# Kernel tuning notes

Hardware: AMD Instinct MI355X
Metric: run time of the kernel (lower is better)

The kernel has to match this reference:

```python
import jax, jax.numpy as jnp
import numpy as np

NUM_HEADS = 12
HEAD_DIM = 64
NPT = 1  # num_prefix_tokens

def _rot(x):
    # pairs (x0,x1) -> (-x1, x0), matching timm's rot()
    x2 = x.reshape(*x.shape[:-1], -1, 2)
    r = jnp.stack([-x2[..., 1], x2[..., 0]], axis=-1)
    return r.reshape(x.shape)

def _apply_rope_cat(x, rope):
    # rope: [N_rot, 2*hd] = sin||cos concatenated
    sin, cos = jnp.split(rope, 2, axis=-1)
    return x * cos + _rot(x) * sin

def setup_inputs() -> dict:
    key = jax.random.key(0)
    ks = jax.random.split(key, 7)
    B, N, C = 8, 4097, 768
    hd = HEAD_DIM
    x = jax.random.normal(ks[0], (B, N, C), jnp.float32)
    rope = jax.random.normal(ks[1], (N - NPT, 2 * hd), jnp.float32)
    qkv_w = jax.random.normal(ks[2], (3 * C, C), jnp.float32) * (C ** -0.5)
    q_bias = jax.random.normal(ks[3], (C,), jnp.float32) * 0.02
    v_bias = jax.random.normal(ks[4], (C,), jnp.float32) * 0.02
    proj_w = jax.random.normal(ks[5], (C, C), jnp.float32) * (C ** -0.5)
    proj_b = jax.random.normal(ks[6], (C,), jnp.float32) * 0.02
    return dict(x=x, rope=rope, qkv_w=qkv_w, q_bias=q_bias, v_bias=v_bias,
                proj_w=proj_w, proj_b=proj_b)

def reference(x, rope, qkv_w, q_bias, v_bias, proj_w, proj_b):
    B, N, C = x.shape
    H, hd = NUM_HEADS, HEAD_DIM
    # fused QKV with k_bias fixed at zero (non-trainable buffer)
    bias = jnp.concatenate([q_bias, jnp.zeros_like(q_bias), v_bias])
    qkv = x @ qkv_w.T + bias                            # [B,N,3C]
    qkv = qkv.reshape(B, N, 3, H, hd).transpose(2, 0, 3, 1, 4)
    q, k, v = qkv[0], qkv[1], qkv[2]                    # [B,H,N,hd]
    # RoPE on all tokens except the prefix (CLS) token
    q = jnp.concatenate([q[:, :, :NPT], _apply_rope_cat(q[:, :, NPT:], rope)], axis=2)
    k = jnp.concatenate([k[:, :, :NPT], _apply_rope_cat(k[:, :, NPT:], rope)], axis=2)
    # linear attention: kv = K^T V, then Q @ kv, normalized by hd*N
    kv = jnp.einsum('bhnd,bhne->bhde', k, v)            # [B,H,hd,hd]
    out = jnp.einsum('bhnd,bhde->bhne', q, kv) / hd / N # [B,H,N,hd]
    out = out.transpose(0, 2, 1, 3).reshape(B, N, C)
    return out @ proj_w.T + proj_b
```

## Files before the change

kernel.cpp:

```cpp
#include <hip/hip_runtime.h>
#include <hip/hip_bf16.h>

typedef __attribute__((ext_vector_type(8))) short short8;
typedef __attribute__((ext_vector_type(4))) float f32x4;

#define B_    8
#define N_    4097
#define C_    768
#define M_TOT (B_*N_)
#define K3    (3*C_)
#define CHUNKS 16
#define NSTEP 24

__device__ __forceinline__ float bf2f(unsigned short u) {
  union { unsigned int i; float f; } x; x.i = ((unsigned int)u) << 16; return x.f;
}
__device__ __forceinline__ unsigned short f2bf(float f) {
  union { float f; unsigned int i; } x; x.f = f;
  unsigned int i = x.i + 0x7fffu + ((x.i >> 16) & 1u);
  return (unsigned short)(i >> 16);
}
__device__ __forceinline__ void gload16(const void* g, void* l) {
  __builtin_amdgcn_global_load_lds(
      (const __attribute__((address_space(1))) void*)g,
      (__attribute__((address_space(3))) void*)l, 16, 0, 0);
}

__global__ __launch_bounds__(256) void cvt_kernel(const float* __restrict__ inx,
                                                  unsigned short* __restrict__ outx,
                                                  const float* __restrict__ inw,
                                                  unsigned short* __restrict__ outw,
                                                  long n4x, long n4tot) {
  long i = (long)blockIdx.x * blockDim.x + threadIdx.x;
  long stride = (long)gridDim.x * blockDim.x;
  for (; i < n4tot; i += stride) {
    const float4* src; ushort4* dst; long j;
    if (i < n4x) { src = (const float4*)inx; dst = (ushort4*)outx; j = i; }
    else         { src = (const float4*)inw; dst = (ushort4*)outw; j = i - n4x; }
    float4 v = src[j];
    ushort4 o;
    o.x = f2bf(v.x); o.y = f2bf(v.y); o.z = f2bf(v.z); o.w = f2bf(v.w);
    dst[j] = o;
  }
}

__global__ __launch_bounds__(512, 4) void gemm_qkv_rope(
    const unsigned short* __restrict__ A,
    const unsigned short* __restrict__ Bw,
    const float* __restrict__ rope,
    const float* __restrict__ qb,
    const float* __restrict__ vb,
    unsigned short* __restrict__ qkv)
{
  __shared__ __align__(16) char L[3*24576];
  const int tid  = threadIdx.x;
  const int wave = tid >> 6, lane = tid & 63;
  const int lr = lane & 15, lk = lane >> 4;
  const int wm = wave >> 2, wn = wave & 3;

  const int o = blockIdx.x;
  const int xcd = o & 7, loc = o >> 3;
  const int tile = (xcd < 1 ? xcd*290 : 290 + (xcd-1)*289) + loc;
  const int m0 = (tile % 257) * 128;
  const int n0 = (tile / 257) * 256;

  const int arow = tid >> 2, achk = tid & 3;
  const int am = min(m0 + arow, M_TOT-1);
  const unsigned short* gA  = A  + (long)am*768 + achk*8;
  const unsigned short* gB1 = Bw + (long)(n0 + arow)*768 + achk*8;
  const unsigned short* gB2 = Bw + (long)(n0 + arow + 128)*768 + achk*8;
  const int dA  = wave*1024;
  const int dB1 = 8192  + wave*1024;
  const int dB2 = 16384 + wave*1024;

  const int abase = (wm*64 + lr)*64 + lk*16;
  const int bbase = 8192 + (wn*64 + lr)*64 + lk*16;

  f32x4 acc[4][4];
#pragma unroll
  for (int i = 0; i < 4; ++i)
#pragma unroll
    for (int j = 0; j < 4; ++j) acc[i][j] = (f32x4){0.f,0.f,0.f,0.f};

  auto STAGE = [&](int buf, int kk) {
    char* sb = L + buf*24576;
    gload16(gA  + kk, sb + dA);
    gload16(gB1 + kk, sb + dB1);
    gload16(gB2 + kk, sb + dB2);
  };
  auto COMPUTE = [&](int buf) {
    const char* sb = L + buf*24576;
    short8 af[4], bfr[4];
#pragma unroll
    for (int mi = 0; mi < 4; ++mi)
      af[mi] = *(const short8*)(sb + abase + mi*1024);
#pragma unroll
    for (int ni = 0; ni < 4; ++ni)
      bfr[ni] = *(const short8*)(sb + bbase + ni*1024);
#pragma unroll
    for (int mi = 0; mi < 4; ++mi)
#pragma unroll
      for (int ni = 0; ni < 4; ++ni)
        acc[mi][ni] = __builtin_amdgcn_mfma_f32_16x16x32_bf16(af[mi], bfr[ni], acc[mi][ni], 0, 0, 0);
  };

  STAGE(0, 0);
  STAGE(1, 32);
  asm volatile("s_waitcnt vmcnt(3)" ::: "memory");
  __builtin_amdgcn_s_barrier();
  __builtin_amdgcn_sched_barrier(0);

  int cur = 0;
  for (int tt = 0; tt < NSTEP-2; ++tt) {
    int stg = cur + 2; if (stg >= 3) stg -= 3;
    STAGE(stg, (tt+2)*32);
    COMPUTE(cur);
    asm volatile("s_waitcnt vmcnt(3)" ::: "memory");
    __builtin_amdgcn_sched_barrier(0);
    __builtin_amdgcn_s_barrier();
    __builtin_amdgcn_sched_barrier(0);
    cur = (cur + 1 == 3) ? 0 : cur + 1;
  }
  COMPUTE(cur);
  asm volatile("s_waitcnt vmcnt(0)" ::: "memory");
  __builtin_amdgcn_sched_barrier(0);
  __builtin_amdgcn_s_barrier();
  __builtin_amdgcn_sched_barrier(0);
  cur = (cur + 1 == 3) ? 0 : cur + 1;
  COMPUTE(cur);

  const int which = n0 / 768;
  unsigned short* plane = qkv + (long)which*M_TOT*768;

  float biasv[4]; int withv[4]; int dv[4];
#pragma unroll
  for (int ni = 0; ni < 4; ++ni) {
    const int gc = n0 + wn*64 + ni*16 + lr;
    const int within = gc - which*768;
    withv[ni] = within;
    dv[ni] = within & 63;
    biasv[ni] = (which == 0) ? qb[within] : (which == 2 ? vb[within] : 0.f);
  }

  if (which == 2) {
#pragma unroll
    for (int mi = 0; mi < 4; ++mi)
#pragma unroll
      for (int r = 0; r < 4; ++r) {
        const int gm = m0 + wm*64 + mi*16 + lk*4 + r;
        if (gm < M_TOT) {
#pragma unroll
          for (int ni = 0; ni < 4; ++ni)
            plane[(long)gm*768 + withv[ni]] = f2bf(acc[mi][ni][r] + biasv[ni]);
        }
      }
  } else {
#pragma unroll
    for (int mi = 0; mi < 4; ++mi) {
#pragma unroll
      for (int r = 0; r < 4; ++r) {
        const int gm = m0 + wm*64 + mi*16 + lk*4 + r;
        const int ntok = gm % 4097;
        const bool valid = gm < M_TOT;
        const bool dorope = (ntok > 0) && valid;
        const float* rp = rope + (long)(ntok - 1)*128;
#pragma unroll
        for (int ni = 0; ni < 4; ++ni) {
          float v = acc[mi][ni][r] + biasv[ni];
          float pair = __shfl_xor(v, 1);
          float vo = v;
          if (dorope) {
            const float s = rp[dv[ni]], c = rp[64 + dv[ni]];
            const float rot = (dv[ni] & 1) ? pair : -pair;
            vo = v*c + rot*s;
          }
          if (valid) plane[(long)gm*768 + withv[ni]] = f2bf(vo);
        }
      }
    }
  }
}

__global__ __launch_bounds__(256) void kv_partial_kernel(
    const unsigned short* __restrict__ qkv, float* __restrict__ part)
{
  const int bh = blockIdx.y;
  const int b = bh / 12, h = bh % 12;
  const int chunk = blockIdx.x;
  const int per = (N_ + CHUNKS - 1) / CHUNKS;
  const int nst = chunk * per;
  const int nen = min(nst + per, N_);
  const unsigned short* Kpl = qkv + (long)M_TOT*768 + ((long)b*N_)*768 + h*64;
  const unsigned short* Vpl = qkv + (long)2*M_TOT*768 + ((long)b*N_)*768 + h*64;
  __shared__ unsigned short Kl[32*64];
  __shared__ unsigned short Vl[32*64];
  const int t = threadIdx.x;
  const int ty = t >> 4, tx = t & 15;
  const int lrow = t >> 3, lpc = t & 7;
  float acc[4][4] = {};
  for (int nb = nst; nb < nen; nb += 32) {
    const int cnt = min(32, nen - nb);
    __syncthreads();
    if (lrow < cnt) {
      *(uint4*)(Kl + lrow*64 + lpc*8) = *(const uint4*)(Kpl + (long)(nb + lrow)*768 + lpc*8);
      *(uint4*)(Vl + lrow*64 + lpc*8) = *(const uint4*)(Vpl + (long)(nb + lrow)*768 + lpc*8);
    }
    __syncthreads();
#pragma unroll 2
    for (int i = 0; i < cnt; ++i) {
      const ushort4 ku = *(const ushort4*)(Kl + i*64 + ty*4);
      const ushort4 vu = *(const ushort4*)(Vl + i*64 + tx*4);
      float kf[4] = {bf2f(ku.x), bf2f(ku.y), bf2f(ku.z), bf2f(ku.w)};
      float vf[4] = {bf2f(vu.x), bf2f(vu.y), bf2f(vu.z), bf2f(vu.w)};
#pragma unroll
      for (int a = 0; a < 4; ++a)
#pragma unroll
        for (int e = 0; e < 4; ++e) acc[a][e] += kf[a]*vf[e];
    }
  }
  float* dst = part + ((long)chunk*96 + bh)*4096 + (ty*4)*64 + tx*4;
#pragma unroll
  for (int a = 0; a < 4; ++a)
#pragma unroll
    for (int e = 0; e < 4; ++e) dst[a*64 + e] = acc[a][e];
}

__global__ __launch_bounds__(256) void mcomb_kernel(const float* __restrict__ part,
                                                    const float* __restrict__ pw,
                                                    unsigned short* __restrict__ McT) {
  const int blk = blockIdx.x;
  const int cs = blk & 1;
  const int h  = (blk >> 1) % 12;
  const int b  = blk / 24;
  const int bh = b*12 + h;
  __shared__ float kvs[64][65];
  const int t = threadIdx.x;
  const int d_own = t >> 2;
  const int eg = (t & 3) * 16;

  float4 a0 = {0,0,0,0}, a1 = {0,0,0,0}, a2 = {0,0,0,0}, a3 = {0,0,0,0};
  const float4* p4 = (const float4*)part;
#pragma unroll
  for (int ch = 0; ch < CHUNKS; ++ch) {
    const long base = ((long)ch*96 + bh)*1024 + d_own*16 + (t & 3)*4;
    float4 v0 = p4[base+0], v1 = p4[base+1], v2 = p4[base+2], v3 = p4[base+3];
    a0.x += v0.x; a0.y += v0.y; a0.z += v0.z; a0.w += v0.w;
    a1.x += v1.x; a1.y += v1.y; a1.z += v1.z; a1.w += v1.w;
    a2.x += v2.x; a2.y += v2.y; a2.z += v2.z; a2.w += v2.w;
    a3.x += v3.x; a3.y += v3.y; a3.z += v3.z; a3.w += v3.w;
  }
  kvs[eg+ 0][d_own] = a0.x; kvs[eg+ 1][d_own] = a0.y; kvs[eg+ 2][d_own] = a0.z; kvs[eg+ 3][d_own] = a0.w;
  kvs[eg+ 4][d_own] = a1.x; kvs[eg+ 5][d_own] = a1.y; kvs[eg+ 6][d_own] = a1.z; kvs[eg+ 7][d_own] = a1.w;
  kvs[eg+ 8][d_own] = a2.x; kvs[eg+ 9][d_own] = a2.y; kvs[eg+10][d_own] = a2.z; kvs[eg+11][d_own] = a2.w;
  kvs[eg+12][d_own] = a3.x; kvs[eg+13][d_own] = a3.y; kvs[eg+14][d_own] = a3.z; kvs[eg+15][d_own] = a3.w;
  __syncthreads();

  const int lane = t & 63;
  const int w    = t >> 6;
  float kvcol[64];
#pragma unroll
  for (int e = 0; e < 64; ++e) kvcol[e] = kvs[e][lane];

  const float scale = (float)(1.0/(64.0*4097.0));
  const int cbase = cs*384 + w*96;
  for (int i = 0; i < 96; ++i) {
    const int c = cbase + i;
    const float* pwrow = pw + (long)c*768 + h*64;
    float s = 0.f;
#pragma unroll
    for (int e = 0; e < 64; ++e) s += pwrow[e] * kvcol[e];
    McT[((long)b*768 + c)*768 + h*64 + lane] = f2bf(s * scale);
  }
}

__global__ __launch_bounds__(512, 4) void gemm_final(
    const unsigned short* __restrict__ qkv,
    const unsigned short* __restrict__ McT,
    const float* __restrict__ pb,
    float* __restrict__ out)
{
  __shared__ __align__(16) char L[3*24576];
  const int tid  = threadIdx.x;
  const int wave = tid >> 6, lane = tid & 63;
  const int lr = lane & 15, lk = lane >> 4;
  const int wm = wave >> 2, wn = wave & 3;

  const int o = blockIdx.x;
  const int xcd = o & 7, loc = o >> 3;
  const int b  = xcd;
  const int ct = loc / 33, mt = loc % 33;
  const int m0 = mt * 128;
  const int c0 = ct * 256;

  const int arow = tid >> 2, achk = tid & 3;
  const int am = min(m0 + arow, N_-1);
  const unsigned short* gA  = qkv + ((long)b*N_ + am)*768 + achk*8;
  const unsigned short* Bb  = McT + (long)b*768*768;
  const unsigned short* gB1 = Bb + (long)(c0 + arow)*768 + achk*8;
  const unsigned short* gB2 = Bb + (long)(c0 + arow + 128)*768 + achk*8;
  const int dA  = wave*1024;
  const int dB1 = 8192  + wave*1024;
  const int dB2 = 16384 + wave*1024;

  const int abase = (wm*64 + lr)*64 + lk*16;
  const int bbase = 8192 + (wn*64 + lr)*64 + lk*16;

  f32x4 acc[4][4];
#pragma unroll
  for (int i = 0; i < 4; ++i)
#pragma unroll
    for (int j = 0; j < 4; ++j) acc[i][j] = (f32x4){0.f,0.f,0.f,0.f};

  auto STAGE = [&](int buf, int kk) {
    char* sb = L + buf*24576;
    gload16(gA  + kk, sb + dA);
    gload16(gB1 + kk, sb + dB1);
    gload16(gB2 + kk, sb + dB2);
  };
  auto COMPUTE = [&](int buf) {
    const char* sb = L + buf*24576;
    short8 af[4], bfr[4];
#pragma unroll
    for (int mi = 0; mi < 4; ++mi)
      af[mi] = *(const short8*)(sb + abase + mi*1024);
#pragma unroll
    for (int ni = 0; ni < 4; ++ni)
      bfr[ni] = *(const short8*)(sb + bbase + ni*1024);
#pragma unroll
    for (int mi = 0; mi < 4; ++mi)
#pragma unroll
      for (int ni = 0; ni < 4; ++ni)
        acc[mi][ni] = __builtin_amdgcn_mfma_f32_16x16x32_bf16(af[mi], bfr[ni], acc[mi][ni], 0, 0, 0);
  };

  STAGE(0, 0);
  STAGE(1, 32);
  asm volatile("s_waitcnt vmcnt(3)" ::: "memory");
  __builtin_amdgcn_s_barrier();
  __builtin_amdgcn_sched_barrier(0);

  int cur = 0;
  for (int tt = 0; tt < NSTEP-2; ++tt) {
    int stg = cur + 2; if (stg >= 3) stg -= 3;
    STAGE(stg, (tt+2)*32);
    COMPUTE(cur);
    asm volatile("s_waitcnt vmcnt(3)" ::: "memory");
    __builtin_amdgcn_sched_barrier(0);
    __builtin_amdgcn_s_barrier();
    __builtin_amdgcn_sched_barrier(0);
    cur = (cur + 1 == 3) ? 0 : cur + 1;
  }
  COMPUTE(cur);
  asm volatile("s_waitcnt vmcnt(0)" ::: "memory");
  __builtin_amdgcn_sched_barrier(0);
  __builtin_amdgcn_s_barrier();
  __builtin_amdgcn_sched_barrier(0);
  cur = (cur + 1 == 3) ? 0 : cur + 1;
  COMPUTE(cur);

#pragma unroll
  for (int mi = 0; mi < 4; ++mi) {
#pragma unroll
    for (int ni = 0; ni < 4; ++ni) {
      const int gc = c0 + wn*64 + ni*16 + lr;
      const float bias = pb[gc];
#pragma unroll
      for (int r = 0; r < 4; ++r) {
        const int tok = m0 + wm*64 + mi*16 + lk*4 + r;
        if (tok < N_)
          out[((long)b*N_ + tok)*768 + gc] = acc[mi][ni][r] + bias;
      }
    }
  }
}

extern "C" void kernel_launch(void* const* d_in, const int* in_sizes, int n_in,
                              void* d_out, int out_size, void* d_ws, size_t ws_size,
                              hipStream_t stream) {
  const float* x      = (const float*)d_in[0];
  const float* rope   = (const float*)d_in[1];
  const float* qkv_w  = (const float*)d_in[2];
  const float* q_bias = (const float*)d_in[3];
  const float* v_bias = (const float*)d_in[4];
  const float* proj_w = (const float*)d_in[5];
  const float* proj_b = (const float*)d_in[6];
  float* out = (float*)d_out;

  char* w0 = (char*)d_ws;
  unsigned short* x_bf  = (unsigned short*)w0;
  unsigned short* wq_bf = (unsigned short*)(w0 + 50343936);
  unsigned short* qkv   = (unsigned short*)(w0 + 50343936 + 3538944);
  float*          part  = (float*)w0;
  unsigned short* McT   = (unsigned short*)(w0 + 25165824 + 1572864);

  const long n4x = (long)M_TOT*768/4;
  const long n4w = (long)K3*768/4;
  cvt_kernel<<<2048, 256, 0, stream>>>(x, x_bf, qkv_w, wq_bf, n4x, n4x + n4w);

  gemm_qkv_rope<<<2313, 512, 0, stream>>>(x_bf, wq_bf, rope, q_bias, v_bias, qkv);

  kv_partial_kernel<<<dim3(CHUNKS, 96), 256, 0, stream>>>(qkv, part);
  mcomb_kernel<<<192, 256, 0, stream>>>(part, proj_w, McT);

  gemm_final<<<792, 512, 0, stream>>>(qkv, McT, proj_b, out);
}
```

Before: 438.1 us.

## Reorder GEMM tile rasterization, double-buffer kv_partial loads, split mcomb wider

```diff
diff --git a/kernel.cpp b/kernel.cpp
--- a/kernel.cpp
+++ b/kernel.cpp
@@ -61,8 +61,8 @@
   const int o = blockIdx.x;
   const int xcd = o & 7, loc = o >> 3;
   const int tile = (xcd < 1 ? xcd*290 : 290 + (xcd-1)*289) + loc;
-  const int m0 = (tile % 257) * 128;
-  const int n0 = (tile / 257) * 256;
+  const int m0 = (tile / 9) * 128;
+  const int n0 = (tile % 9) * 256;
 
   const int arow = tid >> 2, achk = tid & 3;
   const int am = min(m0 + arow, M_TOT-1);
@@ -192,24 +192,37 @@
   const int nen = min(nst + per, N_);
   const unsigned short* Kpl = qkv + (long)M_TOT*768 + ((long)b*N_)*768 + h*64;
   const unsigned short* Vpl = qkv + (long)2*M_TOT*768 + ((long)b*N_)*768 + h*64;
-  __shared__ unsigned short Kl[32*64];
-  __shared__ unsigned short Vl[32*64];
+  __shared__ unsigned short Kl[2][32*64];
+  __shared__ unsigned short Vl[2][32*64];
   const int t = threadIdx.x;
   const int ty = t >> 4, tx = t & 15;
   const int lrow = t >> 3, lpc = t & 7;
   float acc[4][4] = {};
+
+  {
+    const int cnt0 = min(32, nen - nst);
+    if (lrow < cnt0) {
+      *(uint4*)(Kl[0] + lrow*64 + lpc*8) = *(const uint4*)(Kpl + (long)(nst + lrow)*768 + lpc*8);
+      *(uint4*)(Vl[0] + lrow*64 + lpc*8) = *(const uint4*)(Vpl + (long)(nst + lrow)*768 + lpc*8);
+    }
+  }
+  int cur = 0;
   for (int nb = nst; nb < nen; nb += 32) {
+    uint4 kn, vn; int cntn = 0;
+    const int nxt = nb + 32;
+    if (nxt < nen) {
+      cntn = min(32, nen - nxt);
+      if (lrow < cntn) {
+        kn = *(const uint4*)(Kpl + (long)(nxt + lrow)*768 + lpc*8);
+        vn = *(const uint4*)(Vpl + (long)(nxt + lrow)*768 + lpc*8);
+      }
+    }
+    __syncthreads();
     const int cnt = min(32, nen - nb);
-    __syncthreads();
-    if (lrow < cnt) {
-      *(uint4*)(Kl + lrow*64 + lpc*8) = *(const uint4*)(Kpl + (long)(nb + lrow)*768 + lpc*8);
-      *(uint4*)(Vl + lrow*64 + lpc*8) = *(const uint4*)(Vpl + (long)(nb + lrow)*768 + lpc*8);
-    }
-    __syncthreads();
 #pragma unroll 2
     for (int i = 0; i < cnt; ++i) {
-      const ushort4 ku = *(const ushort4*)(Kl + i*64 + ty*4);
-      const ushort4 vu = *(const ushort4*)(Vl + i*64 + tx*4);
+      const ushort4 ku = *(const ushort4*)(Kl[cur] + i*64 + ty*4);
+      const ushort4 vu = *(const ushort4*)(Vl[cur] + i*64 + tx*4);
       float kf[4] = {bf2f(ku.x), bf2f(ku.y), bf2f(ku.z), bf2f(ku.w)};
       float vf[4] = {bf2f(vu.x), bf2f(vu.y), bf2f(vu.z), bf2f(vu.w)};
 #pragma unroll
@@ -217,6 +230,12 @@
 #pragma unroll
         for (int e = 0; e < 4; ++e) acc[a][e] += kf[a]*vf[e];
     }
+    __syncthreads();
+    if (nxt < nen && lrow < cntn) {
+      *(uint4*)(Kl[cur^1] + lrow*64 + lpc*8) = kn;
+      *(uint4*)(Vl[cur^1] + lrow*64 + lpc*8) = vn;
+    }
+    cur ^= 1;
   }
   float* dst = part + ((long)chunk*96 + bh)*4096 + (ty*4)*64 + tx*4;
 #pragma unroll
@@ -229,9 +248,9 @@
                                                     const float* __restrict__ pw,
                                                     unsigned short* __restrict__ McT) {
   const int blk = blockIdx.x;
-  const int cs = blk & 1;
-  const int h  = (blk >> 1) % 12;
-  const int b  = blk / 24;
+  const int cs = blk & 3;
+  const int h  = (blk >> 2) % 12;
+  const int b  = blk / 48;
   const int bh = b*12 + h;
   __shared__ float kvs[64][65];
   const int t = threadIdx.x;
@@ -262,8 +281,8 @@
   for (int e = 0; e < 64; ++e) kvcol[e] = kvs[e][lane];
 
   const float scale = (float)(1.0/(64.0*4097.0));
-  const int cbase = cs*384 + w*96;
-  for (int i = 0; i < 96; ++i) {
+  const int cbase = cs*192 + w*48;
+  for (int i = 0; i < 48; ++i) {
     const int c = cbase + i;
     const float* pwrow = pw + (long)c*768 + h*64;
     float s = 0.f;
@@ -288,7 +307,7 @@
   const int o = blockIdx.x;
   const int xcd = o & 7, loc = o >> 3;
   const int b  = xcd;
-  const int ct = loc / 33, mt = loc % 33;
+  const int mt = loc / 3, ct = loc % 3;
   const int m0 = mt * 128;
   const int c0 = ct * 256;
 
@@ -400,7 +419,7 @@
   gemm_qkv_rope<<<2313, 512, 0, stream>>>(x_bf, wq_bf, rope, q_bias, v_bias, qkv);
 
   kv_partial_kernel<<<dim3(CHUNKS, 96), 256, 0, stream>>>(qkv, part);
-  mcomb_kernel<<<192, 256, 0, stream>>>(part, proj_w, McT);
+  mcomb_kernel<<<384, 256, 0, stream>>>(part, proj_w, McT);
 
   gemm_final<<<792, 512, 0, stream>>>(qkv, McT, proj_b, out);
 }
```

New measurement: 397.0 us. 1.1x faster.
